# Kernel optimization log

Measured on AMD Instinct MI355X. Metric: run time of the kernel, lower is better.

Reference implementation:

```python
import jax, jax.numpy as jnp
import numpy as np

CH = 512
NH = 8
EPS = 1e-5

def setup_inputs() -> dict:
    key = jax.random.key(0)
    ks = jax.random.split(key, 7)
    x = jax.random.normal(ks[0], (1, CH, 64, 64), dtype=jnp.float32)
    norm_w = jnp.ones((CH,), jnp.float32)
    norm_b = jnp.zeros((CH,), jnp.float32)
    s1 = 1.0 / np.sqrt(CH)
    qkv_w = jax.random.uniform(ks[1], (3 * CH, CH), jnp.float32, -s1, s1)
    qkv_b = jax.random.uniform(ks[2], (3 * CH,), jnp.float32, -s1, s1)
    proj_w = jax.random.uniform(ks[3], (CH, CH), jnp.float32, -s1, s1)
    proj_b = jax.random.uniform(ks[4], (CH,), jnp.float32, -s1, s1)
    return {"x": x, "norm_w": norm_w, "norm_b": norm_b, "qkv_w": qkv_w,
            "qkv_b": qkv_b, "proj_w": proj_w, "proj_b": proj_b}

def _forward(x, norm_w, norm_b, qkv_w, qkv_b, proj_w, proj_b):
    B, C, H, W = x.shape
    G = 32
    # GroupNorm(32, C) + SiLU
    xg = x.reshape(B, G, C // G, H, W)
    mu = jnp.mean(xg, axis=(2, 3, 4), keepdims=True)
    var = jnp.var(xg, axis=(2, 3, 4), keepdims=True)
    h = ((xg - mu) * jax.lax.rsqrt(var + EPS)).reshape(B, C, H, W)
    h = h * norm_w[None, :, None, None] + norm_b[None, :, None, None]
    h = jax.nn.silu(h)
    N = H * W
    h = h.reshape(B, C, N)
    # qkv 1x1 conv == channel matmul
    qkv = jnp.einsum('oc,bcn->bon', qkv_w, h) + qkv_b[None, :, None]
    q, k, v = jnp.split(qkv, 3, axis=1)  # each (B, C, N)
    d = C // NH
    # faithful to torch: transpose(1,2) then row-major reshape
    q = q.transpose(0, 2, 1).reshape(B * NH, N, d)
    k = k.transpose(0, 2, 1).reshape(B * NH, N, d)
    v = v.transpose(0, 2, 1).reshape(B * NH, N, d)
    scale = d ** (-0.5)
    attn = jax.nn.softmax(jnp.einsum('bnd,bmd->bnm', q, k) * scale, axis=-1)
    out = jnp.einsum('bnm,bmd->bnd', attn, v)
    out = out.reshape(B, N, C).transpose(0, 2, 1)  # (B, C, N)
    out = jnp.einsum('oc,bcn->bon', proj_w, out) + proj_b[None, :, None]
    return x + out.reshape(B, C, H, W)

def reference(x, norm_w, norm_b, qkv_w, qkv_b, proj_w, proj_b):
    return _forward(x, norm_w, norm_b, qkv_w, qkv_b, proj_w, proj_b)
```

## Files before the change

kernel.cpp:

```cpp
#include <hip/hip_runtime.h>

typedef __attribute__((ext_vector_type(8)))  short s16x8;
typedef __attribute__((ext_vector_type(4)))  float f32x4;
typedef __attribute__((ext_vector_type(16))) float f32x16;
typedef __attribute__((ext_vector_type(4)))  unsigned int u32x4;

#define CHN 512
#define NSP 4096

__device__ __forceinline__ ushort f2b(float f){
  unsigned u = __builtin_bit_cast(unsigned, f);
  u = (u + 0x7fffu + ((u >> 16) & 1u)) >> 16;
  return (ushort)u;
}

__device__ __forceinline__ s16x8 ldfrag(const void* p){
  return *reinterpret_cast<const s16x8*>(p);
}

__device__ __forceinline__ f32x4 mfma16(s16x8 a, s16x8 b, f32x4 c){
  return __builtin_amdgcn_mfma_f32_16x16x32_bf16(a, b, c, 0, 0, 0);
}
__device__ __forceinline__ f32x16 mfma32(s16x8 a, s16x8 b, f32x16 c){
  return __builtin_amdgcn_mfma_f32_32x32x16_bf16(a, b, c, 0, 0, 0);
}
__device__ __forceinline__ unsigned cvtpk(float lo, float hi){
  unsigned r;
  asm("v_cvt_pk_bf16_f32 %0, %1, %2" : "=v"(r) : "v"(lo), "v"(hi));
  return r;
}
__device__ __forceinline__ void gload16(const void* g, void* l){
  __builtin_amdgcn_global_load_lds(
      (const __attribute__((address_space(1))) unsigned int*)g,
      (__attribute__((address_space(3))) unsigned int*)l, 16, 0, 0);
}
__device__ __forceinline__ ushort4 f4b(float4 v){
  ushort4 o;
  o.x = f2b(v.x); o.y = f2b(v.y); o.z = f2b(v.z); o.w = f2b(v.w);
  return o;
}

__global__ __launch_bounds__(256) void prep(const float4* __restrict__ qkvw, const float4* __restrict__ projw,
                                            const float* __restrict__ x,
                                            ushort4* __restrict__ Wq, ushort4* __restrict__ Wp,
                                            float* __restrict__ part){
  int b = blockIdx.x;
  if (b < 768){
    int i = b*256 + threadIdx.x;
    Wq[i] = f4b(qkvw[i]);
  } else if (b < 1024){
    int i = (b-768)*256 + threadIdx.x;
    Wp[i] = f4b(projw[i]);
  } else {
    int pb = b - 1024;
    const float4* p = reinterpret_cast<const float4*>(x + (size_t)pb * 8192);
    float s = 0.f, s2 = 0.f;
    #pragma unroll
    for (int i = 0; i < 8; ++i){
      float4 v = p[threadIdx.x + i*256];
      s  += v.x + v.y + v.z + v.w;
      s2 += v.x*v.x + v.y*v.y + v.z*v.z + v.w*v.w;
    }
    #pragma unroll
    for (int off = 32; off > 0; off >>= 1){ s += __shfl_down(s, off); s2 += __shfl_down(s2, off); }
    __shared__ float ls[4], ls2[4];
    int wv = threadIdx.x >> 6;
    if ((threadIdx.x & 63) == 0){ ls[wv] = s; ls2[wv] = s2; }
    __syncthreads();
    if (threadIdx.x == 0){
      part[pb*2]     = ls[0]+ls[1]+ls[2]+ls[3];
      part[pb*2 + 1] = ls2[0]+ls2[1]+ls2[2]+ls2[3];
    }
  }
}

__global__ __launch_bounds__(64) void gn_final(const float* __restrict__ part, float* __restrict__ stat){
  int g = threadIdx.x;
  if (g < 32){
    float s = 0.f, s2 = 0.f;
    #pragma unroll
    for (int i = 0; i < 8; ++i){ s += part[(g*8+i)*2]; s2 += part[(g*8+i)*2+1]; }
    float mu  = s * (1.f/65536.f);
    float var = s2 * (1.f/65536.f) - mu*mu;
    stat[g]      = mu;
    stat[32 + g] = rsqrtf(var + 1e-5f);
  }
}

__global__ __launch_bounds__(256) void norm_apply(const float* __restrict__ x, const float* __restrict__ stat,
                                                  const float* __restrict__ nw, const float* __restrict__ nb,
                                                  ushort* __restrict__ h_t){
  __shared__ float tile[64][65];
  int ct0 = (blockIdx.x >> 6) << 6;
  int nt0 = (blockIdx.x & 63) << 6;
  int tc = threadIdx.x >> 6;
  int tn = threadIdx.x & 63;
  #pragma unroll
  for (int rr = 0; rr < 16; ++rr){
    int cl = rr*4 + tc;
    int c  = ct0 + cl;
    float v  = x[(size_t)c * NSP + nt0 + tn];
    float hn = (v - stat[c >> 4]) * stat[32 + (c >> 4)] * nw[c] + nb[c];
    float sv = hn / (1.f + __expf(-hn));
    tile[tn][cl] = sv;
  }
  __syncthreads();
  #pragma unroll
  for (int rr = 0; rr < 16; ++rr){
    int nl = rr*4 + tc;
    h_t[(size_t)(nt0 + nl) * CHN + ct0 + tn] = f2b(tile[nl][tn]);
  }
}

template<int MODE, int BM, int BN>
__global__ __launch_bounds__(256) void gemm_tn(
    const ushort* __restrict__ A, const ushort* __restrict__ Bw,
    const float* __restrict__ bias, const float* __restrict__ xres,
    ushort* __restrict__ qS, ushort* __restrict__ kF, ushort* __restrict__ vF,
    float* __restrict__ outF)
{
  constexpr int RW = BM/2, CW = BN/2;
  constexpr int MI = RW/16, NJ = CW/16;
  __shared__ __align__(16) ushort As[2][BM*32];
  __shared__ __align__(16) ushort Bs[2][BN*32];
  int tid = threadIdx.x;
  int lane = tid & 63, wv = tid >> 6;
  int lr = lane & 15, lg = lane >> 4;
  int wr = wv >> 1, wc = wv & 1;
  int nbB = blockIdx.x * BM;
  int obB = blockIdx.y * BN;
  int nb = nbB + wr*RW, ob = obB + wc*CW;
  f32x4 acc[MI][NJ] = {};

  const ushort* Ag = A  + (size_t)(nbB + (tid>>2))*CHN + (tid&3)*8;
  const ushort* Bg = Bw + (size_t)(obB + (tid>>2))*CHN + (tid&3)*8;

  #define GSTAGE(BUF, KK) {                                                    \
    _Pragma("unroll") for (int ii = 0; ii < BM/64; ++ii)                       \
      gload16(Ag + (size_t)ii*64*CHN + (KK), &As[BUF][ii*2048 + tid*8]);       \
    _Pragma("unroll") for (int ii = 0; ii < BN/64; ++ii)                       \
      gload16(Bg + (size_t)ii*64*CHN + (KK), &Bs[BUF][ii*2048 + tid*8]); }

  GSTAGE(0, 0);
  asm volatile("s_waitcnt vmcnt(0)" ::: "memory");
  __syncthreads();
  int cur = 0;
  for (int kk = 0; kk < CHN; kk += 32){
    if (kk < CHN-32) GSTAGE(cur^1, kk+32);
    s16x8 af[MI], bf[NJ];
    #pragma unroll
    for (int t = 0; t < MI; ++t) af[t] = *(const s16x8*)&As[cur][(wr*RW + lr + t*16)*32 + lg*8];
    #pragma unroll
    for (int t = 0; t < NJ; ++t) bf[t] = *(const s16x8*)&Bs[cur][(wc*CW + lr + t*16)*32 + lg*8];
    #pragma unroll
    for (int i = 0; i < MI; ++i)
      #pragma unroll
      for (int j = 0; j < NJ; ++j)
        acc[i][j] = mfma16(af[i], bf[j], acc[i][j]);
    asm volatile("s_waitcnt vmcnt(0)" ::: "memory");
    __syncthreads();
    cur ^= 1;
  }
  #undef GSTAGE

  if (MODE == 0){
    #pragma unroll
    for (int j = 0; j < NJ; ++j){
      int o = ob + j*16 + lr;
      float bs = bias[o];
      int sec = o >> 9;
      int co  = o & 511;
      int bb = co >> 6, dd = co & 63;
      if (sec == 0){
        const float qsc = 0.18033688011112042f;
        #pragma unroll
        for (int i = 0; i < MI; ++i){
          int n0 = nb + i*16 + lg*4;
          int hh = n0 >> 9, aa = n0 & 511;
          size_t base = ((size_t)((hh<<3)+bb)*512 + aa)*64 + dd;
          #pragma unroll
          for (int r = 0; r < 4; ++r)
            qS[base + (size_t)r*64] = f2b((acc[i][j][r] + bs) * qsc);
        }
      } else if (sec == 1){
        int s = dd >> 4, khi = (dd >> 3) & 1, off = dd & 7;
        #pragma unroll
        for (int i = 0; i < MI; ++i){
          int n0 = nb + i*16 + lg*4;
          int hh = n0 >> 9, aa = n0 & 511;
          int T = bb*16 + (aa >> 5);
          size_t widx = ((((size_t)hh*128 + T)*4 + s)*64 + (aa & 31) + 32*khi)*8 + off;
          #pragma unroll
          for (int r = 0; r < 4; ++r)
            kF[widx + (size_t)r*8] = f2b(acc[i][j][r] + bs);
        }
      } else {
        int l31v = dd & 31, fh = dd >> 5;
        #pragma unroll
        for (int i = 0; i < MI; ++i){
          int n0 = nb + i*16 + lg*4;
          int hh = n0 >> 9, aa = n0 & 511;
          int T = bb*16 + (aa >> 5);
          int w = aa & 31;
          int f = fh*2 + (w >> 4);
          int vhi = (w >> 3) & 1, koff = w & 7;
          size_t widx = ((((size_t)hh*128 + T)*4 + f)*64 + l31v + 32*vhi)*8 + koff;
          ushort4 pk;
          pk.x = f2b(acc[i][j][0] + bs);
          pk.y = f2b(acc[i][j][1] + bs);
          pk.z = f2b(acc[i][j][2] + bs);
          pk.w = f2b(acc[i][j][3] + bs);
          *reinterpret_cast<ushort4*>(vF + widx) = pk;
        }
      }
    }
  } else {
    #pragma unroll
    for (int j = 0; j < NJ; ++j){
      int o = ob + j*16 + lr;
      float bs = bias[o];
      #pragma unroll
      for (int i = 0; i < MI; ++i){
        int n0 = nb + i*16 + lg*4;
        f32x4 xr = *reinterpret_cast<const f32x4*>(xres + (size_t)o*NSP + n0);
        f32x4 ov;
        #pragma unroll
        for (int r = 0; r < 4; ++r) ov[r] = acc[i][j][r] + bs + xr[r];
        *reinterpret_cast<f32x4*>(outF + (size_t)o*NSP + n0) = ov;
      }
    }
  }
}

__global__ __launch_bounds__(512, 4) void flash7(
    const ushort* __restrict__ qS, const ushort* __restrict__ kF,
    const ushort* __restrict__ vF, ushort* __restrict__ attnT)
{
  __shared__ __align__(16) ushort ldsKV[4][2][4096];
  __shared__ __align__(16) float w4buf[2][32];
  __shared__ __align__(16) float llds[3][64];
  int lane = threadIdx.x & 63, wv = threadIdx.x >> 6;
  int l31 = lane & 31, hi = lane >> 5;
  int qg = wv & 1, kvh = wv >> 1;
  int bx = (blockIdx.x & 7) * 64 + (blockIdx.x >> 3);
  int hh    = bx >> 6;
  int b1    = (bx >> 3) & 7;
  int chunk = bx & 7;
  int a0 = chunk * 64 + qg * 32;

  const ushort* qp = qS + ((size_t)((hh*8 + b1)*512) + a0 + l31)*64 + hi*8;
  s16x8 qf0 = ldfrag(qp), qf1 = ldfrag(qp+16), qf2 = ldfrag(qp+32), qf3 = ldfrag(qp+48);

  f32x16 O0 = {}, O1 = {};
  f32x4 lacc = {};

  #define COMPUTE(K0,K1,K2,K3, V0,V1,V2,V3) {                                  \
    f32x16 S = {};                                                             \
    S = mfma32(K0, qf0, S); S = mfma32(K1, qf1, S);                            \
    S = mfma32(K2, qf2, S); S = mfma32(K3, qf3, S);                            \
    float p[16];                                                               \
    _Pragma("unroll") for (int r = 0; r < 16; ++r)                             \
      p[r] = __builtin_amdgcn_exp2f(S[r]);                                     \
    lacc[0] += (p[0]+p[1])   + (p[2]+p[3]);                                    \
    lacc[1] += (p[4]+p[5])   + (p[6]+p[7]);                                    \
    lacc[2] += (p[8]+p[9])   + (p[10]+p[11]);                                  \
    lacc[3] += (p[12]+p[13]) + (p[14]+p[15]);                                  \
    unsigned A0 = cvtpk(p[0],p[1]),  A1 = cvtpk(p[2],p[3]);                    \
    unsigned B0 = cvtpk(p[4],p[5]),  B1 = cvtpk(p[6],p[7]);                    \
    asm("v_permlane32_swap_b32 %0, %1" : "+v"(A0), "+v"(B0));                  \
    asm("v_permlane32_swap_b32 %0, %1" : "+v"(A1), "+v"(B1));                  \
    unsigned C0 = cvtpk(p[8],p[9]),  C1 = cvtpk(p[10],p[11]);                  \
    unsigned D0 = cvtpk(p[12],p[13]),D1 = cvtpk(p[14],p[15]);                  \
    asm("v_permlane32_swap_b32 %0, %1" : "+v"(C0), "+v"(D0));                  \
    asm("v_permlane32_swap_b32 %0, %1" : "+v"(C1), "+v"(D1));                  \
    u32x4 w1 = {A0, A1, B0, B1}, w2 = {C0, C1, D0, D1};                        \
    s16x8 pa1 = __builtin_bit_cast(s16x8, w1);                                 \
    s16x8 pa2 = __builtin_bit_cast(s16x8, w2);                                 \
    O0 = mfma32(pa1, V0, O0); O0 = mfma32(pa2, V1, O0);                        \
    O1 = mfma32(pa1, V2, O1); O1 = mfma32(pa2, V3, O1);                        \
  }

  #define STAGE(BUF, T) {                                                      \
    size_t off_ = (size_t)hh*262144 + (size_t)(T)*2048 + (qg*64 + lane)*8;     \
    const ushort* ks_ = kF + off_;                                             \
    const ushort* vs_ = vF + off_;                                             \
    ushort* lk_ = &ldsKV[kvh][BUF][(qg*64 + lane)*8];                          \
    gload16(ks_,        lk_);                                                  \
    gload16(ks_ + 1024, lk_ + 1024);                                           \
    gload16(vs_,        lk_ + 2048);                                           \
    gload16(vs_ + 1024, lk_ + 2048 + 1024); }

  int cur = 0;
  STAGE(0, kvh*32);
  asm volatile("s_waitcnt vmcnt(0)" ::: "memory");
  __syncthreads();

  for (int t2 = 0; t2 < 32; ++t2){
    if (t2 < 31) STAGE(cur ^ 1, kvh*32 + t2 + 1);
    const ushort* kc = &ldsKV[kvh][cur][lane*8];
    s16x8 k0 = *(const s16x8*)(kc +    0), k1 = *(const s16x8*)(kc +  512);
    s16x8 k2 = *(const s16x8*)(kc + 1024), k3 = *(const s16x8*)(kc + 1536);
    s16x8 v0 = *(const s16x8*)(kc + 2048), v1 = *(const s16x8*)(kc + 2560);
    s16x8 v2 = *(const s16x8*)(kc + 3072), v3 = *(const s16x8*)(kc + 3584);
    COMPUTE(k0,k1,k2,k3, v0,v1,v2,v3);
    asm volatile("s_waitcnt vmcnt(0)" ::: "memory");
    __syncthreads();
    cur ^= 1;
  }

  float ts = (lacc[0]+lacc[1]) + (lacc[2]+lacc[3]);
  float tu = ts, tv = ts;
  asm("v_permlane32_swap_b32 %0, %1" : "+v"(tu), "+v"(tv));
  float lrun = tu + tv;

  float* fb = reinterpret_cast<float*>(&ldsKV[0][0][0]);
  if (kvh < 3){
    #pragma unroll
    for (int g = 0; g < 4; ++g)
      #pragma unroll
      for (int r4 = 0; r4 < 4; ++r4){
        int row = g*8 + hi*4 + r4;
        fb[((kvh*64) + qg*32 + row)*68 + l31]      = O0[g*4+r4];
        fb[((kvh*64) + qg*32 + row)*68 + l31 + 32] = O1[g*4+r4];
      }
    if (hi == 0) llds[kvh][qg*32 + l31] = lrun;
  }
  __syncthreads();
  if (kvh == 3){
    if (hi == 0){
      int idx = qg*32 + l31;
      float lt = llds[0][idx] + llds[1][idx] + llds[2][idx] + lrun;
      w4buf[qg][l31] = 1.0f / lt;
    }
    asm volatile("s_waitcnt lgkmcnt(0)" ::: "memory");
    size_t colBase = (size_t)b1*64 + l31;
    #pragma unroll
    for (int g = 0; g < 4; ++g){
      f32x4 iv = *reinterpret_cast<const f32x4*>(&w4buf[qg][g*8 + hi*4]);
      #pragma unroll
      for (int r4 = 0; r4 < 4; ++r4){
        int row = g*8 + hi*4 + r4;
        int fr = qg*32 + row;
        float o0 = (fb[(fr)*68 + l31]      + fb[(64 + fr)*68 + l31]
                  + fb[(128 + fr)*68 + l31]      + O0[g*4+r4]) * iv[r4];
        float o1 = (fb[(fr)*68 + l31 + 32] + fb[(64 + fr)*68 + l31 + 32]
                  + fb[(128 + fr)*68 + l31 + 32] + O1[g*4+r4]) * iv[r4];
        size_t base = ((size_t)(hh*512 + a0 + row))*CHN + colBase;
        attnT[base]      = f2b(o0);
        attnT[base + 32] = f2b(o1);
      }
    }
  }
  #undef STAGE
  #undef COMPUTE
}

extern "C" void kernel_launch(void* const* d_in, const int* in_sizes, int n_in,
                              void* d_out, int out_size, void* d_ws, size_t ws_size,
                              hipStream_t stream)
{
  (void)in_sizes; (void)n_in; (void)out_size; (void)ws_size;
  const float* x     = (const float*)d_in[0];
  const float* normw = (const float*)d_in[1];
  const float* normb = (const float*)d_in[2];
  const float* qkvw  = (const float*)d_in[3];
  const float* qkvb  = (const float*)d_in[4];
  const float* projw = (const float*)d_in[5];
  const float* projb = (const float*)d_in[6];
  float* out = (float*)d_out;

  char* w = (char*)d_ws;
  float*  stat = (float*)w;
  ushort* h_t  = (ushort*)(w + 1024);
  ushort* Wq   = (ushort*)(w + 1024 + 4194304);
  ushort* Wp   = (ushort*)(w + 1024 + 4194304 + 1572864);
  ushort* qSb  = (ushort*)(w + 1024 + 4194304 + 1572864 + 524288);
  ushort* kFb  = qSb + 2097152;
  ushort* vFb  = kFb + 2097152;
  ushort* attnT = h_t;
  float* part  = (float*)h_t;

  prep<<<1280, 256, 0, stream>>>((const float4*)qkvw, (const float4*)projw, x,
                                 (ushort4*)Wq, (ushort4*)Wp, part);
  gn_final<<<1, 64, 0, stream>>>(part, stat);
  norm_apply<<<512, 256, 0, stream>>>(x, stat, normw, normb, h_t);
  gemm_tn<0,128,128><<<dim3(32, 12), 256, 0, stream>>>(h_t, Wq, qkvb, nullptr, qSb, kFb, vFb, nullptr);
  flash7<<<512, 512, 0, stream>>>(qSb, kFb, vFb, attnT);
  gemm_tn<1,64,64><<<dim3(64, 8), 256, 0, stream>>>(attnT, Wp, projb, x, nullptr, nullptr, nullptr, out);
}
```

Before: 84.87 us.

## Fold GroupNorm finalize into norm_apply and register-stage KV in flash kernel

The single-block gn_final launch is removed; every norm_apply block now recomputes the 32 group statistics from the partial sums into shared memory. The partial-sum buffer moves to its own workspace slot so it no longer aliases h_t. The attention kernel drops the LDS double-buffered K/V staging and its per-tile barriers. Instead each wave handles 64 query rows with two Q fragment sets, reusing each K/V fragment for both, and loads K/V directly from global into registers with a two-deep software prefetch. This raises register pressure and halves the threads per block. K/V reads now go straight to global or cache, with no LDS sharing across waves.

```diff
diff --git a/kernel.cpp b/kernel.cpp
--- a/kernel.cpp
+++ b/kernel.cpp
@@ -74,23 +74,22 @@
   }
 }
 
-__global__ __launch_bounds__(64) void gn_final(const float* __restrict__ part, float* __restrict__ stat){
-  int g = threadIdx.x;
-  if (g < 32){
+__global__ __launch_bounds__(256) void norm_apply(const float* __restrict__ x, const float* __restrict__ part,
+                                                  const float* __restrict__ nw, const float* __restrict__ nb,
+                                                  ushort* __restrict__ h_t){
+  __shared__ float tile[64][65];
+  __shared__ float smu[32], srs[32];
+  if (threadIdx.x < 32){
+    int g = threadIdx.x;
     float s = 0.f, s2 = 0.f;
     #pragma unroll
     for (int i = 0; i < 8; ++i){ s += part[(g*8+i)*2]; s2 += part[(g*8+i)*2+1]; }
     float mu  = s * (1.f/65536.f);
     float var = s2 * (1.f/65536.f) - mu*mu;
-    stat[g]      = mu;
-    stat[32 + g] = rsqrtf(var + 1e-5f);
-  }
-}
-
-__global__ __launch_bounds__(256) void norm_apply(const float* __restrict__ x, const float* __restrict__ stat,
-                                                  const float* __restrict__ nw, const float* __restrict__ nb,
-                                                  ushort* __restrict__ h_t){
-  __shared__ float tile[64][65];
+    smu[g] = mu;
+    srs[g] = rsqrtf(var + 1e-5f);
+  }
+  __syncthreads();
   int ct0 = (blockIdx.x >> 6) << 6;
   int nt0 = (blockIdx.x & 63) << 6;
   int tc = threadIdx.x >> 6;
@@ -100,7 +99,7 @@
     int cl = rr*4 + tc;
     int c  = ct0 + cl;
     float v  = x[(size_t)c * NSP + nt0 + tn];
-    float hn = (v - stat[c >> 4]) * stat[32 + (c >> 4)] * nw[c] + nb[c];
+    float hn = (v - smu[c >> 4]) * srs[c >> 4] * nw[c] + nb[c];
     float sv = hn / (1.f + __expf(-hn));
     tile[tn][cl] = sv;
   }
@@ -232,127 +231,151 @@
   }
 }
 
-__global__ __launch_bounds__(512, 4) void flash7(
+__global__ __launch_bounds__(256) void flash8(
     const ushort* __restrict__ qS, const ushort* __restrict__ kF,
     const ushort* __restrict__ vF, ushort* __restrict__ attnT)
 {
-  __shared__ __align__(16) ushort ldsKV[4][2][4096];
-  __shared__ __align__(16) float w4buf[2][32];
-  __shared__ __align__(16) float llds[3][64];
-  int lane = threadIdx.x & 63, wv = threadIdx.x >> 6;
+  __shared__ __align__(16) float fb[3][64][68];
+  __shared__ float llds[3][64];
+  __shared__ float winv[64];
+  int lane = threadIdx.x & 63, kvh = threadIdx.x >> 6;
   int l31 = lane & 31, hi = lane >> 5;
-  int qg = wv & 1, kvh = wv >> 1;
   int bx = (blockIdx.x & 7) * 64 + (blockIdx.x >> 3);
   int hh    = bx >> 6;
   int b1    = (bx >> 3) & 7;
   int chunk = bx & 7;
-  int a0 = chunk * 64 + qg * 32;
-
-  const ushort* qp = qS + ((size_t)((hh*8 + b1)*512) + a0 + l31)*64 + hi*8;
-  s16x8 qf0 = ldfrag(qp), qf1 = ldfrag(qp+16), qf2 = ldfrag(qp+32), qf3 = ldfrag(qp+48);
-
-  f32x16 O0 = {}, O1 = {};
-  f32x4 lacc = {};
-
-  #define COMPUTE(K0,K1,K2,K3, V0,V1,V2,V3) {                                  \
-    f32x16 S = {};                                                             \
-    S = mfma32(K0, qf0, S); S = mfma32(K1, qf1, S);                            \
-    S = mfma32(K2, qf2, S); S = mfma32(K3, qf3, S);                            \
-    float p[16];                                                               \
+  int a0 = chunk * 64;
+
+  const ushort* qpA = qS + ((size_t)((hh*8 + b1)*512) + a0 + l31)*64 + hi*8;
+  const ushort* qpB = qpA + 32*64;
+  s16x8 qA0 = ldfrag(qpA), qA1 = ldfrag(qpA+16), qA2 = ldfrag(qpA+32), qA3 = ldfrag(qpA+48);
+  s16x8 qB0 = ldfrag(qpB), qB1 = ldfrag(qpB+16), qB2 = ldfrag(qpB+32), qB3 = ldfrag(qpB+48);
+
+  f32x16 OA0 = {}, OA1 = {}, OB0 = {}, OB1 = {};
+  f32x4 laccA = {}, laccB = {};
+
+  size_t base0 = (size_t)hh*262144 + (size_t)(kvh*32)*2048 + lane*8;
+
+  #define LOADKV(T, K0,K1,K2,K3, V0,V1,V2,V3) {                                \
+    const ushort* kp_ = kF + base0 + (size_t)(T)*2048;                         \
+    const ushort* vp_ = vF + base0 + (size_t)(T)*2048;                         \
+    K0 = ldfrag(kp_);        K1 = ldfrag(kp_ + 512);                           \
+    K2 = ldfrag(kp_ + 1024); K3 = ldfrag(kp_ + 1536);                          \
+    V0 = ldfrag(vp_);        V1 = ldfrag(vp_ + 512);                           \
+    V2 = ldfrag(vp_ + 1024); V3 = ldfrag(vp_ + 1536); }
+
+  #define COMPUTE64(K0,K1,K2,K3, V0,V1,V2,V3) {                                \
+    f32x16 SA = {}, SB = {};                                                   \
+    SA = mfma32(K0, qA0, SA); SA = mfma32(K1, qA1, SA);                        \
+    SA = mfma32(K2, qA2, SA); SA = mfma32(K3, qA3, SA);                        \
+    SB = mfma32(K0, qB0, SB); SB = mfma32(K1, qB1, SB);                        \
+    SB = mfma32(K2, qB2, SB); SB = mfma32(K3, qB3, SB);                        \
+    float pA[16], pB[16];                                                      \
     _Pragma("unroll") for (int r = 0; r < 16; ++r)                             \
-      p[r] = __builtin_amdgcn_exp2f(S[r]);                                     \
-    lacc[0] += (p[0]+p[1])   + (p[2]+p[3]);                                    \
-    lacc[1] += (p[4]+p[5])   + (p[6]+p[7]);                                    \
-    lacc[2] += (p[8]+p[9])   + (p[10]+p[11]);                                  \
-    lacc[3] += (p[12]+p[13]) + (p[14]+p[15]);                                  \
-    unsigned A0 = cvtpk(p[0],p[1]),  A1 = cvtpk(p[2],p[3]);                    \
-    unsigned B0 = cvtpk(p[4],p[5]),  B1 = cvtpk(p[6],p[7]);                    \
-    asm("v_permlane32_swap_b32 %0, %1" : "+v"(A0), "+v"(B0));                  \
-    asm("v_permlane32_swap_b32 %0, %1" : "+v"(A1), "+v"(B1));                  \
-    unsigned C0 = cvtpk(p[8],p[9]),  C1 = cvtpk(p[10],p[11]);                  \
-    unsigned D0 = cvtpk(p[12],p[13]),D1 = cvtpk(p[14],p[15]);                  \
-    asm("v_permlane32_swap_b32 %0, %1" : "+v"(C0), "+v"(D0));                  \
-    asm("v_permlane32_swap_b32 %0, %1" : "+v"(C1), "+v"(D1));                  \
-    u32x4 w1 = {A0, A1, B0, B1}, w2 = {C0, C1, D0, D1};                        \
-    s16x8 pa1 = __builtin_bit_cast(s16x8, w1);                                 \
-    s16x8 pa2 = __builtin_bit_cast(s16x8, w2);                                 \
-    O0 = mfma32(pa1, V0, O0); O0 = mfma32(pa2, V1, O0);                        \
-    O1 = mfma32(pa1, V2, O1); O1 = mfma32(pa2, V3, O1);                        \
-  }
-
-  #define STAGE(BUF, T) {                                                      \
-    size_t off_ = (size_t)hh*262144 + (size_t)(T)*2048 + (qg*64 + lane)*8;     \
-    const ushort* ks_ = kF + off_;                                             \
-    const ushort* vs_ = vF + off_;                                             \
-    ushort* lk_ = &ldsKV[kvh][BUF][(qg*64 + lane)*8];                          \
-    gload16(ks_,        lk_);                                                  \
-    gload16(ks_ + 1024, lk_ + 1024);                                           \
-    gload16(vs_,        lk_ + 2048);                                           \
-    gload16(vs_ + 1024, lk_ + 2048 + 1024); }
-
-  int cur = 0;
-  STAGE(0, kvh*32);
-  asm volatile("s_waitcnt vmcnt(0)" ::: "memory");
-  __syncthreads();
-
-  for (int t2 = 0; t2 < 32; ++t2){
-    if (t2 < 31) STAGE(cur ^ 1, kvh*32 + t2 + 1);
-    const ushort* kc = &ldsKV[kvh][cur][lane*8];
-    s16x8 k0 = *(const s16x8*)(kc +    0), k1 = *(const s16x8*)(kc +  512);
-    s16x8 k2 = *(const s16x8*)(kc + 1024), k3 = *(const s16x8*)(kc + 1536);
-    s16x8 v0 = *(const s16x8*)(kc + 2048), v1 = *(const s16x8*)(kc + 2560);
-    s16x8 v2 = *(const s16x8*)(kc + 3072), v3 = *(const s16x8*)(kc + 3584);
-    COMPUTE(k0,k1,k2,k3, v0,v1,v2,v3);
-    asm volatile("s_waitcnt vmcnt(0)" ::: "memory");
-    __syncthreads();
-    cur ^= 1;
-  }
-
-  float ts = (lacc[0]+lacc[1]) + (lacc[2]+lacc[3]);
-  float tu = ts, tv = ts;
-  asm("v_permlane32_swap_b32 %0, %1" : "+v"(tu), "+v"(tv));
-  float lrun = tu + tv;
-
-  float* fb = reinterpret_cast<float*>(&ldsKV[0][0][0]);
+      pA[r] = __builtin_amdgcn_exp2f(SA[r]);                                   \
+    laccA[0] += (pA[0]+pA[1])   + (pA[2]+pA[3]);                               \
+    laccA[1] += (pA[4]+pA[5])   + (pA[6]+pA[7]);                               \
+    laccA[2] += (pA[8]+pA[9])   + (pA[10]+pA[11]);                             \
+    laccA[3] += (pA[12]+pA[13]) + (pA[14]+pA[15]);                             \
+    unsigned aA0 = cvtpk(pA[0],pA[1]),  aA1 = cvtpk(pA[2],pA[3]);              \
+    unsigned bA0 = cvtpk(pA[4],pA[5]),  bA1 = cvtpk(pA[6],pA[7]);              \
+    asm("v_permlane32_swap_b32 %0, %1" : "+v"(aA0), "+v"(bA0));                \
+    asm("v_permlane32_swap_b32 %0, %1" : "+v"(aA1), "+v"(bA1));                \
+    unsigned cA0 = cvtpk(pA[8],pA[9]),  cA1 = cvtpk(pA[10],pA[11]);            \
+    unsigned dA0 = cvtpk(pA[12],pA[13]),dA1 = cvtpk(pA[14],pA[15]);            \
+    asm("v_permlane32_swap_b32 %0, %1" : "+v"(cA0), "+v"(dA0));                \
+    asm("v_permlane32_swap_b32 %0, %1" : "+v"(cA1), "+v"(dA1));                \
+    u32x4 wA1 = {aA0, aA1, bA0, bA1}, wA2 = {cA0, cA1, dA0, dA1};              \
+    s16x8 paA1 = __builtin_bit_cast(s16x8, wA1);                               \
+    s16x8 paA2 = __builtin_bit_cast(s16x8, wA2);                               \
+    OA0 = mfma32(paA1, V0, OA0); OA0 = mfma32(paA2, V1, OA0);                  \
+    OA1 = mfma32(paA1, V2, OA1); OA1 = mfma32(paA2, V3, OA1);                  \
+    _Pragma("unroll") for (int r = 0; r < 16; ++r)                             \
+      pB[r] = __builtin_amdgcn_exp2f(SB[r]);                                   \
+    laccB[0] += (pB[0]+pB[1])   + (pB[2]+pB[3]);                               \
+    laccB[1] += (pB[4]+pB[5])   + (pB[6]+pB[7]);                               \
+    laccB[2] += (pB[8]+pB[9])   + (pB[10]+pB[11]);                             \
+    laccB[3] += (pB[12]+pB[13]) + (pB[14]+pB[15]);                             \
+    unsigned aB0 = cvtpk(pB[0],pB[1]),  aB1 = cvtpk(pB[2],pB[3]);              \
+    unsigned bB0 = cvtpk(pB[4],pB[5]),  bB1 = cvtpk(pB[6],pB[7]);              \
+    asm("v_permlane32_swap_b32 %0, %1" : "+v"(aB0), "+v"(bB0));                \
+    asm("v_permlane32_swap_b32 %0, %1" : "+v"(aB1), "+v"(bB1));                \
+    unsigned cB0 = cvtpk(pB[8],pB[9]),  cB1 = cvtpk(pB[10],pB[11]);            \
+    unsigned dB0 = cvtpk(pB[12],pB[13]),dB1 = cvtpk(pB[14],pB[15]);            \
+    asm("v_permlane32_swap_b32 %0, %1" : "+v"(cB0), "+v"(dB0));                \
+    asm("v_permlane32_swap_b32 %0, %1" : "+v"(cB1), "+v"(dB1));                \
+    u32x4 wB1 = {aB0, aB1, bB0, bB1}, wB2 = {cB0, cB1, dB0, dB1};              \
+    s16x8 paB1 = __builtin_bit_cast(s16x8, wB1);                               \
+    s16x8 paB2 = __builtin_bit_cast(s16x8, wB2);                               \
+    OB0 = mfma32(paB1, V0, OB0); OB0 = mfma32(paB2, V1, OB0);                  \
+    OB1 = mfma32(paB1, V2, OB1); OB1 = mfma32(paB2, V3, OB1);                  \
+  }
+
+  s16x8 kA0,kA1,kA2,kA3, vA0,vA1,vA2,vA3;
+  s16x8 kB0,kB1,kB2,kB3, vB0,vB1,vB2,vB3;
+  LOADKV(0, kA0,kA1,kA2,kA3, vA0,vA1,vA2,vA3);
+  for (int t2 = 0; t2 < 32; t2 += 2){
+    LOADKV(t2+1, kB0,kB1,kB2,kB3, vB0,vB1,vB2,vB3);
+    COMPUTE64(kA0,kA1,kA2,kA3, vA0,vA1,vA2,vA3);
+    if (t2 + 2 < 32) LOADKV(t2+2, kA0,kA1,kA2,kA3, vA0,vA1,vA2,vA3);
+    COMPUTE64(kB0,kB1,kB2,kB3, vB0,vB1,vB2,vB3);
+  }
+
+  float tsA = (laccA[0]+laccA[1]) + (laccA[2]+laccA[3]);
+  float tuA = tsA, tvA = tsA;
+  asm("v_permlane32_swap_b32 %0, %1" : "+v"(tuA), "+v"(tvA));
+  float lrunA = tuA + tvA;
+  float tsB = (laccB[0]+laccB[1]) + (laccB[2]+laccB[3]);
+  float tuB = tsB, tvB = tsB;
+  asm("v_permlane32_swap_b32 %0, %1" : "+v"(tuB), "+v"(tvB));
+  float lrunB = tuB + tvB;
+
   if (kvh < 3){
     #pragma unroll
     for (int g = 0; g < 4; ++g)
       #pragma unroll
       for (int r4 = 0; r4 < 4; ++r4){
         int row = g*8 + hi*4 + r4;
-        fb[((kvh*64) + qg*32 + row)*68 + l31]      = O0[g*4+r4];
-        fb[((kvh*64) + qg*32 + row)*68 + l31 + 32] = O1[g*4+r4];
+        fb[kvh][row][l31]           = OA0[g*4+r4];
+        fb[kvh][row][l31 + 32]      = OA1[g*4+r4];
+        fb[kvh][row + 32][l31]      = OB0[g*4+r4];
+        fb[kvh][row + 32][l31 + 32] = OB1[g*4+r4];
       }
-    if (hi == 0) llds[kvh][qg*32 + l31] = lrun;
+    if (hi == 0){ llds[kvh][l31] = lrunA; llds[kvh][32 + l31] = lrunB; }
   }
   __syncthreads();
   if (kvh == 3){
     if (hi == 0){
-      int idx = qg*32 + l31;
-      float lt = llds[0][idx] + llds[1][idx] + llds[2][idx] + lrun;
-      w4buf[qg][l31] = 1.0f / lt;
+      float ltA = llds[0][l31] + llds[1][l31] + llds[2][l31] + lrunA;
+      float ltB = llds[0][32+l31] + llds[1][32+l31] + llds[2][32+l31] + lrunB;
+      winv[l31]      = 1.0f / ltA;
+      winv[32 + l31] = 1.0f / ltB;
     }
     asm volatile("s_waitcnt lgkmcnt(0)" ::: "memory");
     size_t colBase = (size_t)b1*64 + l31;
     #pragma unroll
     for (int g = 0; g < 4; ++g){
-      f32x4 iv = *reinterpret_cast<const f32x4*>(&w4buf[qg][g*8 + hi*4]);
+      f32x4 ivA = *reinterpret_cast<const f32x4*>(&winv[g*8 + hi*4]);
+      f32x4 ivB = *reinterpret_cast<const f32x4*>(&winv[32 + g*8 + hi*4]);
       #pragma unroll
       for (int r4 = 0; r4 < 4; ++r4){
         int row = g*8 + hi*4 + r4;
-        int fr = qg*32 + row;
-        float o0 = (fb[(fr)*68 + l31]      + fb[(64 + fr)*68 + l31]
-                  + fb[(128 + fr)*68 + l31]      + O0[g*4+r4]) * iv[r4];
-        float o1 = (fb[(fr)*68 + l31 + 32] + fb[(64 + fr)*68 + l31 + 32]
-                  + fb[(128 + fr)*68 + l31 + 32] + O1[g*4+r4]) * iv[r4];
-        size_t base = ((size_t)(hh*512 + a0 + row))*CHN + colBase;
-        attnT[base]      = f2b(o0);
-        attnT[base + 32] = f2b(o1);
+        float o0 = (fb[0][row][l31] + fb[1][row][l31] + fb[2][row][l31] + OA0[g*4+r4]) * ivA[r4];
+        float o1 = (fb[0][row][l31+32] + fb[1][row][l31+32] + fb[2][row][l31+32] + OA1[g*4+r4]) * ivA[r4];
+        int rowB = row + 32;
+        float o2 = (fb[0][rowB][l31] + fb[1][rowB][l31] + fb[2][rowB][l31] + OB0[g*4+r4]) * ivB[r4];
+        float o3 = (fb[0][rowB][l31+32] + fb[1][rowB][l31+32] + fb[2][rowB][l31+32] + OB1[g*4+r4]) * ivB[r4];
+        size_t baseA = ((size_t)(hh*512 + a0 + row))*CHN + colBase;
+        size_t baseB = ((size_t)(hh*512 + a0 + rowB))*CHN + colBase;
+        attnT[baseA]      = f2b(o0);
+        attnT[baseA + 32] = f2b(o1);
+        attnT[baseB]      = f2b(o2);
+        attnT[baseB + 32] = f2b(o3);
       }
     }
   }
-  #undef STAGE
-  #undef COMPUTE
+  #undef LOADKV
+  #undef COMPUTE64
 }
 
 extern "C" void kernel_launch(void* const* d_in, const int* in_sizes, int n_in,
@@ -370,21 +393,19 @@
   float* out = (float*)d_out;
 
   char* w = (char*)d_ws;
-  float*  stat = (float*)w;
   ushort* h_t  = (ushort*)(w + 1024);
   ushort* Wq   = (ushort*)(w + 1024 + 4194304);
   ushort* Wp   = (ushort*)(w + 1024 + 4194304 + 1572864);
   ushort* qSb  = (ushort*)(w + 1024 + 4194304 + 1572864 + 524288);
   ushort* kFb  = qSb + 2097152;
   ushort* vFb  = kFb + 2097152;
+  float*  part = (float*)(vFb + 2097152);
   ushort* attnT = h_t;
-  float* part  = (float*)h_t;
 
   prep<<<1280, 256, 0, stream>>>((const float4*)qkvw, (const float4*)projw, x,
                                  (ushort4*)Wq, (ushort4*)Wp, part);
-  gn_final<<<1, 64, 0, stream>>>(part, stat);
-  norm_apply<<<512, 256, 0, stream>>>(x, stat, normw, normb, h_t);
+  norm_apply<<<512, 256, 0, stream>>>(x, part, normw, normb, h_t);
   gemm_tn<0,128,128><<<dim3(32, 12), 256, 0, stream>>>(h_t, Wq, qkvb, nullptr, qSb, kFb, vFb, nullptr);
-  flash7<<<512, 512, 0, stream>>>(qSb, kFb, vFb, attnT);
+  flash8<<<512, 256, 0, stream>>>(qSb, kFb, vFb, attnT);
   gemm_tn<1,64,64><<<dim3(64, 8), 256, 0, stream>>>(attnT, Wp, projb, x, nullptr, nullptr, nullptr, out);
 }
```

Result: slower. 90.02 us (+6.1%).

## Fuse GN finalize into norm_apply; stream V via registers in flash kernel

Applied to the files above, without the earlier changes.

Removes the single-block gn_final launch by having each norm_apply block recompute the group mean/rstd from the partial sums into shared memory, and moves the partial buffer so it no longer aliases h_t. In the attention kernel, only K is staged through LDS (halving the LDS footprint), while V fragments are loaded straight from global into registers one tile ahead, with a partial vmcnt wait. The cross-wave reduction now parks partial O in bf16 instead of fp32. This trades LDS traffic and footprint (allowing more resident blocks) for extra VGPR pressure and a small precision loss in the partial-sum reduction.

```diff
diff --git a/kernel.cpp b/kernel.cpp
--- a/kernel.cpp
+++ b/kernel.cpp
@@ -12,6 +12,9 @@
   unsigned u = __builtin_bit_cast(unsigned, f);
   u = (u + 0x7fffu + ((u >> 16) & 1u)) >> 16;
   return (ushort)u;
+}
+__device__ __forceinline__ float b2f(ushort u){
+  return __builtin_bit_cast(float, ((unsigned)u) << 16);
 }
 
 __device__ __forceinline__ s16x8 ldfrag(const void* p){
@@ -74,23 +77,22 @@
   }
 }
 
-__global__ __launch_bounds__(64) void gn_final(const float* __restrict__ part, float* __restrict__ stat){
-  int g = threadIdx.x;
-  if (g < 32){
+__global__ __launch_bounds__(256) void norm_apply(const float* __restrict__ x, const float* __restrict__ part,
+                                                  const float* __restrict__ nw, const float* __restrict__ nb,
+                                                  ushort* __restrict__ h_t){
+  __shared__ float tile[64][65];
+  __shared__ float smu[32], srs[32];
+  if (threadIdx.x < 32){
+    int g = threadIdx.x;
     float s = 0.f, s2 = 0.f;
     #pragma unroll
     for (int i = 0; i < 8; ++i){ s += part[(g*8+i)*2]; s2 += part[(g*8+i)*2+1]; }
     float mu  = s * (1.f/65536.f);
     float var = s2 * (1.f/65536.f) - mu*mu;
-    stat[g]      = mu;
-    stat[32 + g] = rsqrtf(var + 1e-5f);
-  }
-}
-
-__global__ __launch_bounds__(256) void norm_apply(const float* __restrict__ x, const float* __restrict__ stat,
-                                                  const float* __restrict__ nw, const float* __restrict__ nb,
-                                                  ushort* __restrict__ h_t){
-  __shared__ float tile[64][65];
+    smu[g] = mu;
+    srs[g] = rsqrtf(var + 1e-5f);
+  }
+  __syncthreads();
   int ct0 = (blockIdx.x >> 6) << 6;
   int nt0 = (blockIdx.x & 63) << 6;
   int tc = threadIdx.x >> 6;
@@ -100,7 +102,7 @@
     int cl = rr*4 + tc;
     int c  = ct0 + cl;
     float v  = x[(size_t)c * NSP + nt0 + tn];
-    float hn = (v - stat[c >> 4]) * stat[32 + (c >> 4)] * nw[c] + nb[c];
+    float hn = (v - smu[c >> 4]) * srs[c >> 4] * nw[c] + nb[c];
     float sv = hn / (1.f + __expf(-hn));
     tile[tn][cl] = sv;
   }
@@ -232,13 +234,13 @@
   }
 }
 
-__global__ __launch_bounds__(512, 4) void flash7(
+__global__ __launch_bounds__(512) void flash9(
     const ushort* __restrict__ qS, const ushort* __restrict__ kF,
     const ushort* __restrict__ vF, ushort* __restrict__ attnT)
 {
-  __shared__ __align__(16) ushort ldsKV[4][2][4096];
-  __shared__ __align__(16) float w4buf[2][32];
+  __shared__ __align__(16) ushort ldsK[4][2][2048];
   __shared__ __align__(16) float llds[3][64];
+  __shared__ __align__(16) float winv[64];
   int lane = threadIdx.x & 63, wv = threadIdx.x >> 6;
   int l31 = lane & 31, hi = lane >> 5;
   int qg = wv & 1, kvh = wv >> 1;
@@ -253,11 +255,28 @@
 
   f32x16 O0 = {}, O1 = {};
   f32x4 lacc = {};
-
-  #define COMPUTE(K0,K1,K2,K3, V0,V1,V2,V3) {                                  \
+  s16x8 v0, v1, v2, v3;
+
+  size_t tbase = (size_t)hh*262144 + (size_t)(kvh*32)*2048;
+
+  #define STAGEK(BUF, T) {                                                     \
+    const ushort* ks_ = kF + tbase + (size_t)(T)*2048 + qg*1024 + lane*8;      \
+    ushort* lk_ = &ldsK[kvh][BUF][qg*1024 + lane*8];                           \
+    gload16(ks_,       lk_);                                                   \
+    gload16(ks_ + 512, lk_ + 512); }
+
+  #define LOADV(T) {                                                           \
+    const ushort* vp_ = vF + tbase + (size_t)(T)*2048 + lane*8;                \
+    v0 = ldfrag(vp_);        v1 = ldfrag(vp_ + 512);                           \
+    v2 = ldfrag(vp_ + 1024); v3 = ldfrag(vp_ + 1536); }
+
+  #define COMPUTE(BUF) {                                                       \
+    const ushort* kc = &ldsK[kvh][BUF][lane*8];                                \
+    s16x8 k0 = *(const s16x8*)(kc),        k1 = *(const s16x8*)(kc +  512);    \
+    s16x8 k2 = *(const s16x8*)(kc + 1024), k3 = *(const s16x8*)(kc + 1536);    \
     f32x16 S = {};                                                             \
-    S = mfma32(K0, qf0, S); S = mfma32(K1, qf1, S);                            \
-    S = mfma32(K2, qf2, S); S = mfma32(K3, qf3, S);                            \
+    S = mfma32(k0, qf0, S); S = mfma32(k1, qf1, S);                            \
+    S = mfma32(k2, qf2, S); S = mfma32(k3, qf3, S);                            \
     float p[16];                                                               \
     _Pragma("unroll") for (int r = 0; r < 16; ++r)                             \
       p[r] = __builtin_amdgcn_exp2f(S[r]);                                     \
@@ -276,52 +295,47 @@
     u32x4 w1 = {A0, A1, B0, B1}, w2 = {C0, C1, D0, D1};                        \
     s16x8 pa1 = __builtin_bit_cast(s16x8, w1);                                 \
     s16x8 pa2 = __builtin_bit_cast(s16x8, w2);                                 \
-    O0 = mfma32(pa1, V0, O0); O0 = mfma32(pa2, V1, O0);                        \
-    O1 = mfma32(pa1, V2, O1); O1 = mfma32(pa2, V3, O1);                        \
-  }
-
-  #define STAGE(BUF, T) {                                                      \
-    size_t off_ = (size_t)hh*262144 + (size_t)(T)*2048 + (qg*64 + lane)*8;     \
-    const ushort* ks_ = kF + off_;                                             \
-    const ushort* vs_ = vF + off_;                                             \
-    ushort* lk_ = &ldsKV[kvh][BUF][(qg*64 + lane)*8];                          \
-    gload16(ks_,        lk_);                                                  \
-    gload16(ks_ + 1024, lk_ + 1024);                                           \
-    gload16(vs_,        lk_ + 2048);                                           \
-    gload16(vs_ + 1024, lk_ + 2048 + 1024); }
-
+    O0 = mfma32(pa1, v0, O0); O0 = mfma32(pa2, v1, O0);                        \
+    O1 = mfma32(pa1, v2, O1); O1 = mfma32(pa2, v3, O1);                        \
+  }
+
+  STAGEK(0, 0);
+  __builtin_amdgcn_sched_barrier(0);
+  LOADV(0);
+  asm volatile("s_waitcnt vmcnt(4)" ::: "memory");
+  __syncthreads();
   int cur = 0;
-  STAGE(0, kvh*32);
-  asm volatile("s_waitcnt vmcnt(0)" ::: "memory");
-  __syncthreads();
-
-  for (int t2 = 0; t2 < 32; ++t2){
-    if (t2 < 31) STAGE(cur ^ 1, kvh*32 + t2 + 1);
-    const ushort* kc = &ldsKV[kvh][cur][lane*8];
-    s16x8 k0 = *(const s16x8*)(kc +    0), k1 = *(const s16x8*)(kc +  512);
-    s16x8 k2 = *(const s16x8*)(kc + 1024), k3 = *(const s16x8*)(kc + 1536);
-    s16x8 v0 = *(const s16x8*)(kc + 2048), v1 = *(const s16x8*)(kc + 2560);
-    s16x8 v2 = *(const s16x8*)(kc + 3072), v3 = *(const s16x8*)(kc + 3584);
-    COMPUTE(k0,k1,k2,k3, v0,v1,v2,v3);
-    asm volatile("s_waitcnt vmcnt(0)" ::: "memory");
+  for (int t = 0; t < 32; ++t){
+    if (t < 31){
+      STAGEK(cur^1, t+1);
+      __builtin_amdgcn_sched_barrier(0);
+    }
+    COMPUTE(cur);
+    if (t < 31){
+      LOADV(t+1);
+      asm volatile("s_waitcnt vmcnt(4)" ::: "memory");
+    }
     __syncthreads();
     cur ^= 1;
   }
+  #undef STAGEK
+  #undef LOADV
+  #undef COMPUTE
 
   float ts = (lacc[0]+lacc[1]) + (lacc[2]+lacc[3]);
   float tu = ts, tv = ts;
   asm("v_permlane32_swap_b32 %0, %1" : "+v"(tu), "+v"(tv));
   float lrun = tu + tv;
 
-  float* fb = reinterpret_cast<float*>(&ldsKV[0][0][0]);
   if (kvh < 3){
+    ushort* park = &ldsK[kvh][0][0];
     #pragma unroll
     for (int g = 0; g < 4; ++g)
       #pragma unroll
       for (int r4 = 0; r4 < 4; ++r4){
-        int row = g*8 + hi*4 + r4;
-        fb[((kvh*64) + qg*32 + row)*68 + l31]      = O0[g*4+r4];
-        fb[((kvh*64) + qg*32 + row)*68 + l31 + 32] = O1[g*4+r4];
+        int fr = qg*32 + g*8 + hi*4 + r4;
+        park[fr*64 + l31]      = f2b(O0[g*4+r4]);
+        park[fr*64 + l31 + 32] = f2b(O1[g*4+r4]);
       }
     if (hi == 0) llds[kvh][qg*32 + l31] = lrun;
   }
@@ -329,30 +343,30 @@
   if (kvh == 3){
     if (hi == 0){
       int idx = qg*32 + l31;
-      float lt = llds[0][idx] + llds[1][idx] + llds[2][idx] + lrun;
-      w4buf[qg][l31] = 1.0f / lt;
+      winv[idx] = 1.0f / (llds[0][idx] + llds[1][idx] + llds[2][idx] + lrun);
     }
     asm volatile("s_waitcnt lgkmcnt(0)" ::: "memory");
+    const ushort* p0 = &ldsK[0][0][0];
+    const ushort* p1 = &ldsK[1][0][0];
+    const ushort* p2 = &ldsK[2][0][0];
     size_t colBase = (size_t)b1*64 + l31;
     #pragma unroll
     for (int g = 0; g < 4; ++g){
-      f32x4 iv = *reinterpret_cast<const f32x4*>(&w4buf[qg][g*8 + hi*4]);
+      f32x4 iv = *reinterpret_cast<const f32x4*>(&winv[qg*32 + g*8 + hi*4]);
       #pragma unroll
       for (int r4 = 0; r4 < 4; ++r4){
         int row = g*8 + hi*4 + r4;
         int fr = qg*32 + row;
-        float o0 = (fb[(fr)*68 + l31]      + fb[(64 + fr)*68 + l31]
-                  + fb[(128 + fr)*68 + l31]      + O0[g*4+r4]) * iv[r4];
-        float o1 = (fb[(fr)*68 + l31 + 32] + fb[(64 + fr)*68 + l31 + 32]
-                  + fb[(128 + fr)*68 + l31 + 32] + O1[g*4+r4]) * iv[r4];
+        float o0 = (b2f(p0[fr*64 + l31]) + b2f(p1[fr*64 + l31])
+                  + b2f(p2[fr*64 + l31]) + O0[g*4+r4]) * iv[r4];
+        float o1 = (b2f(p0[fr*64 + l31 + 32]) + b2f(p1[fr*64 + l31 + 32])
+                  + b2f(p2[fr*64 + l31 + 32]) + O1[g*4+r4]) * iv[r4];
         size_t base = ((size_t)(hh*512 + a0 + row))*CHN + colBase;
         attnT[base]      = f2b(o0);
         attnT[base + 32] = f2b(o1);
       }
     }
   }
-  #undef STAGE
-  #undef COMPUTE
 }
 
 extern "C" void kernel_launch(void* const* d_in, const int* in_sizes, int n_in,
@@ -370,21 +384,19 @@
   float* out = (float*)d_out;
 
   char* w = (char*)d_ws;
-  float*  stat = (float*)w;
   ushort* h_t  = (ushort*)(w + 1024);
   ushort* Wq   = (ushort*)(w + 1024 + 4194304);
   ushort* Wp   = (ushort*)(w + 1024 + 4194304 + 1572864);
   ushort* qSb  = (ushort*)(w + 1024 + 4194304 + 1572864 + 524288);
   ushort* kFb  = qSb + 2097152;
   ushort* vFb  = kFb + 2097152;
+  float*  part = (float*)(vFb + 2097152);
   ushort* attnT = h_t;
-  float* part  = (float*)h_t;
 
   prep<<<1280, 256, 0, stream>>>((const float4*)qkvw, (const float4*)projw, x,
                                  (ushort4*)Wq, (ushort4*)Wp, part);
-  gn_final<<<1, 64, 0, stream>>>(part, stat);
-  norm_apply<<<512, 256, 0, stream>>>(x, stat, normw, normb, h_t);
+  norm_apply<<<512, 256, 0, stream>>>(x, part, normw, normb, h_t);
   gemm_tn<0,128,128><<<dim3(32, 12), 256, 0, stream>>>(h_t, Wq, qkvb, nullptr, qSb, kFb, vFb, nullptr);
-  flash7<<<512, 512, 0, stream>>>(qSb, kFb, vFb, attnT);
+  flash9<<<512, 512, 0, stream>>>(qSb, kFb, vFb, attnT);
   gemm_tn<1,64,64><<<dim3(64, 8), 256, 0, stream>>>(attnT, Wp, projb, x, nullptr, nullptr, nullptr, out);
 }
```

Result: no change. 85.25 us (+0.4%).
